# Performance work log

Hardware: AMD Instinct MI355X
Metric: run time of the kernel (lower is better)

The kernel has to match this reference:

```python
import jax, jax.numpy as jnp
import numpy as np

K = 100  # low-rank dimension


def setup_inputs() -> dict:
    key = jax.random.key(0)
    k1, k2 = jax.random.split(key)
    N, D = 100000, 512
    X = jax.random.normal(k1, (N, D), dtype=jnp.float32)
    # xavier-normal init for Linear(d, 4k): std = sqrt(2/(fan_in+fan_out))
    std = np.sqrt(2.0 / (D + 4 * K)).astype(np.float32)
    W = jax.random.normal(k2, (4 * K, D), dtype=jnp.float32) * std
    b = jnp.zeros((4 * K,), dtype=jnp.float32)
    return {"X": X, "W": W, "b": b}


def reference(X, W, b):
    # tmp = ReLU(X @ W^T + b): [N, 4k]
    tmp = jax.nn.relu(X @ W.T + b)
    U = tmp[:, :K]            # [N, k]
    V = tmp[:, K:2 * K]       # [N, k]
    Z = tmp[:, 2 * K:3 * K]   # [N, k]
    T = tmp[:, 3 * K:]        # [N, k]
    N_rows = X.shape[0]
    # joint_normalize2: sum(U @ (V^T @ ones)) / N + 1e-6 == <colsum(U), colsum(V)> / N + 1e-6
    norm_factor = jnp.dot(jnp.sum(U, axis=0), jnp.sum(V, axis=0)) / N_rows + 1e-6
    Dscale = 1.0 / norm_factor
    # low-rank attention: U @ (V^T @ Z) via small [k, k] intermediate
    VtZ = jnp.einsum('nk,nj->kj', V, Z)   # [k, k]
    res = (U @ VtZ) * Dscale              # [N, k]
    out = jnp.concatenate([res, T], axis=1)  # [N, 2k]
    # dropout p=0.0 (eval-equivalent): identity
    return out
```

## Files before the change

kernel.cpp:

```cpp
#include <hip/hip_runtime.h>
#include <cstdint>

typedef __bf16 bf16;
typedef __attribute__((ext_vector_type(8))) __bf16 bf16x8;
typedef __attribute__((ext_vector_type(4))) __bf16 bf16x4;
typedef __attribute__((ext_vector_type(4))) float f32x4;

#define NROWS 100000
#define DIM   512
#define NC    400
#define NTILE 695

#define WS_WP    0u
#define WS_SUMU  458752u
#define WS_SUMV  459152u
#define WS_DSC   459552u
#define WS_VTZT  459776u
#define WS_U     524288u
#define WS_PART  66124288u
#define WS_SUMP  71041536u
#define WS_NEED  72291936u

__device__ __forceinline__ void gload_lds16(const void* g, void* l) {
  __builtin_amdgcn_global_load_lds(
      (const __attribute__((address_space(1))) uint32_t*)g,
      (__attribute__((address_space(3))) uint32_t*)l,
      16, 0, 0);
}

__global__ void k1_prep(const float* __restrict__ W, bf16* __restrict__ wp,
                        float* __restrict__ sums) {
  const int idx = blockIdx.x * 256 + threadIdx.x;
  if (idx < 200) sums[idx] = 0.f;
  if (idx >= 16 * 4 * 448 * 8) return;
  const int e = idx & 7;
  int r = idx >> 3;
  const int col = r % 448; r /= 448;
  const int g = r & 3;
  const int t = r >> 2;
  const int k = t * 32 + 4 * g + ((e < 4) ? e : (12 + e));
  wp[idx] = (bf16)((col < NC) ? W[col * DIM + k] : 0.f);
}

__global__ __launch_bounds__(768, 3) void k2_main(
    const float* __restrict__ X, const bf16* __restrict__ Wp,
    const float* __restrict__ bias, float* __restrict__ out,
    bf16* __restrict__ U, float* __restrict__ part, float* __restrict__ sumP) {
  __shared__ __align__(16) char pool[141312];
  char* Abase0 = pool;
  char* Bbase0 = pool + 55296;

  const int tid  = threadIdx.x;
  const int lane = tid & 63;
  const int wave = tid >> 6;
  const int wm = wave >> 2;
  const int wn = wave & 3;
  const int m  = lane & 15;
  const int g  = lane >> 4;
  const int rb = blockIdx.x * 144;

  f32x4 acc[3][7];
#pragma unroll
  for (int i = 0; i < 3; ++i)
#pragma unroll
    for (int j = 0; j < 7; ++j) acc[i][j] = (f32x4){0.f, 0.f, 0.f, 0.f};

  const int na  = (wave < 6) ? 2 : 1;
  const int ca0 = (wave < 6) ? wave * 2 : 12 + (wave - 6);
  const size_t swb = (size_t)(((lane & 7) ^ (lane >> 3)) * 16);
  int gr0 = rb + ca0 * 8 + (lane >> 3);       if (gr0 > NROWS - 1) gr0 = NROWS - 1;
  int gr1 = rb + (ca0 + 1) * 8 + (lane >> 3); if (gr1 > NROWS - 1) gr1 = NROWS - 1;
  const char* asrc0 = (const char*)X + (size_t)gr0 * 2048 + swb;
  const char* asrc1 = (const char*)X + (size_t)gr1 * 2048 + swb;
  const int nbc = (wave < 4) ? 3 : 2;
  const int bc0 = (wave < 4) ? wave * 3 : 12 + (wave - 4) * 2;
  const char* wpc = (const char*)Wp;

#define STAGE(T, BUF)                                                          \
  do {                                                                         \
    char* ad = Abase0 + (BUF) * 18432 + ca0 * 1024 + lane * 16;                \
    gload_lds16(asrc0 + (size_t)(T) * 128, ad);                                \
    if (na == 2) gload_lds16(asrc1 + (size_t)(T) * 128, ad + 1024);            \
    const char* bsrc = wpc + (size_t)(T) * 28672;                              \
    for (int q = 0; q < nbc; ++q)                                              \
      gload_lds16(bsrc + (bc0 + q) * 1024 + lane * 16,                         \
                  Bbase0 + (BUF) * 28672 + (bc0 + q) * 1024);                  \
  } while (0)

  STAGE(0, 0);
  STAGE(1, 1);

#pragma unroll
  for (int t = 0; t < 16; ++t) {
    const int cur = t % 3;
    if (t < 15) {
      if (wave < 4)      asm volatile("s_waitcnt vmcnt(5)\n\ts_barrier" ::: "memory");
      else if (wave < 6) asm volatile("s_waitcnt vmcnt(4)\n\ts_barrier" ::: "memory");
      else               asm volatile("s_waitcnt vmcnt(3)\n\ts_barrier" ::: "memory");
    } else {
      asm volatile("s_waitcnt vmcnt(0)\n\ts_barrier" ::: "memory");
    }
    if (t + 2 < 16) STAGE(t + 2, (t + 2) % 3);

    const int sw = (m & 7) * 16;
    const char* abuf = Abase0 + cur * 18432;
    bf16x8 af[3];
#pragma unroll
    for (int mf = 0; mf < 3; ++mf) {
      const char* rowp = abuf + (wm * 48 + mf * 16 + m) * 128;
      f32x4 alo = *(const f32x4*)(rowp + ((16 * g) ^ sw));
      f32x4 ahi = *(const f32x4*)(rowp + ((64 + 16 * g) ^ sw));
      af[mf] = (bf16x8){(bf16)alo.x, (bf16)alo.y, (bf16)alo.z, (bf16)alo.w,
                        (bf16)ahi.x, (bf16)ahi.y, (bf16)ahi.z, (bf16)ahi.w};
    }

    const bf16* Bc = (const bf16*)(Bbase0 + cur * 28672);
    __builtin_amdgcn_s_setprio(1);
#pragma unroll
    for (int nf = 0; nf < 7; ++nf) {
      const int n = wn * 112 + nf * 16 + m;
      bf16x8 bfr = *(const bf16x8*)(Bc + (g * 448 + n) * 8);
#pragma unroll
      for (int mf = 0; mf < 3; ++mf)
        acc[mf][nf] = __builtin_amdgcn_mfma_f32_16x16x32_bf16(af[mf], bfr, acc[mf][nf], 0, 0, 0);
    }
    __builtin_amdgcn_s_setprio(0);
  }
#undef STAGE
  __syncthreads();

  bf16* ldsVZ = (bf16*)pool;
  float* sp   = (float*)(pool + 75264);
  float csum[7];
#pragma unroll
  for (int nf = 0; nf < 7; ++nf) csum[nf] = 0.f;

#pragma unroll
  for (int mf = 0; mf < 3; ++mf) {
#pragma unroll
    for (int nf = 0; nf < 7; ++nf) {
      const int c = wn * 112 + nf * 16 + m;
      const float bv = (c < NC) ? bias[c] : 0.f;
      const int rl0 = wm * 48 + mf * 16 + 4 * g;
      bf16 vz[4];
#pragma unroll
      for (int r = 0; r < 4; ++r) {
        const int row = rb + rl0 + r;
        float v = fmaxf(acc[mf][nf][r] + bv, 0.f);
        const float v2 = (row < NROWS) ? v : 0.f;
        if (row < NROWS) {
          if (c < 100) U[(size_t)row * 128 + c] = (bf16)v;
          if (c >= 300 && c < NC) out[(size_t)row * 200 + 100 + (c - 300)] = v;
        }
        vz[r] = (bf16)v2;
        if (c < 200) csum[nf] += v2;
      }
      if (c >= 100 && c < 300) {
        const int vr = (c < 200) ? (c - 100) : (112 + (c - 200));
        *(bf16x4*)&ldsVZ[(size_t)vr * 168 + rl0] = (bf16x4){vz[0], vz[1], vz[2], vz[3]};
      }
    }
  }
  for (int i = tid; i < 8832; i += 768) {
    int rr, cc;
    if (i < 5376) { rr = i / 24; cc = 144 + (i % 24); }
    else { const int j = i - 5376; const int q = j / 144; cc = j % 144;
           rr = (q < 12) ? (100 + q) : (200 + q); }
    ldsVZ[(size_t)rr * 168 + cc] = (bf16)0.f;
  }
#pragma unroll
  for (int nf = 0; nf < 7; ++nf) {
    float s = csum[nf];
    s += __shfl_xor(s, 16, 64);
    s += __shfl_xor(s, 32, 64);
    if (lane < 16) sp[wave * 112 + nf * 16 + lane] = s;
  }
  __syncthreads();

  if (wave < 7) {
    f32x4 acc2[7];
#pragma unroll
    for (int j = 0; j < 7; ++j) acc2[j] = (f32x4){0.f, 0.f, 0.f, 0.f};
    const bf16* vA = ldsVZ + (size_t)(wave * 16 + m) * 168;
#pragma unroll
    for (int kc = 0; kc < 5; ++kc) {
      bf16x4 a0 = *(const bf16x4*)(vA + kc * 32 + 4 * g);
      bf16x4 a1 = *(const bf16x4*)(vA + kc * 32 + 16 + 4 * g);
      bf16x8 af_ = {a0[0], a0[1], a0[2], a0[3], a1[0], a1[1], a1[2], a1[3]};
#pragma unroll
      for (int fj = 0; fj < 7; ++fj) {
        const bf16* vB = ldsVZ + (size_t)(112 + fj * 16 + m) * 168 + kc * 32;
        bf16x4 b0 = *(const bf16x4*)(vB + 4 * g);
        bf16x4 b1 = *(const bf16x4*)(vB + 16 + 4 * g);
        bf16x8 bf_ = {b0[0], b0[1], b0[2], b0[3], b1[0], b1[1], b1[2], b1[3]};
        acc2[fj] = __builtin_amdgcn_mfma_f32_16x16x32_bf16(af_, bf_, acc2[fj], 0, 0, 0);
      }
    }
    float* pb = part + (size_t)(blockIdx.x % 98) * 12544;
#pragma unroll
    for (int fj = 0; fj < 7; ++fj)
#pragma unroll
      for (int r = 0; r < 4; ++r)
        atomicAdd(&pb[(wave * 16 + 4 * g + r) * 112 + fj * 16 + m], acc2[fj][r]);
  }
  if (tid < 200) {
    const int wq = tid / 112, cc = tid % 112;
    sumP[(size_t)blockIdx.x * 200 + tid] =
        sp[(0 * 4 + wq) * 112 + cc] + sp[(1 * 4 + wq) * 112 + cc] +
        sp[(2 * 4 + wq) * 112 + cc];
  }
}

__global__ void k4a0_redsum(const float* __restrict__ sumP,
                            float* __restrict__ sumU, float* __restrict__ sumV) {
  __shared__ float red[4];
  const int c = blockIdx.x;
  const int tid = threadIdx.x;
  float s = 0.f;
  for (int b = tid; b < NTILE; b += 256) s += sumP[(size_t)b * 200 + c];
#pragma unroll
  for (int off = 1; off < 64; off <<= 1) s += __shfl_xor(s, off, 64);
  if ((tid & 63) == 0) red[tid >> 6] = s;
  __syncthreads();
  if (tid == 0) {
    float t = red[0] + red[1] + red[2] + red[3];
    if (c < 100) sumU[c] = t; else sumV[c - 100] = t;
  }
}

__global__ void k4a_norm(const float* __restrict__ sumU, const float* __restrict__ sumV,
                         float* __restrict__ dsc) {
  const int l = threadIdx.x;
  float v = 0.f;
  if (l < 50) v = sumU[l] * sumV[l] + sumU[l + 50] * sumV[l + 50];
#pragma unroll
  for (int off = 32; off > 0; off >>= 1) v += __shfl_down(v, off, 64);
  if (l == 0) dsc[0] = 1.f / (v * (1.f / (float)NROWS) + 1e-6f);
}

__global__ void k4b_final(const float* __restrict__ part, const float* __restrict__ dsc,
                          bf16* __restrict__ vtzt) {
  const int idx = blockIdx.x * 256 + threadIdx.x;
  if (idx < 1792) vtzt[(idx >> 4) * 128 + 112 + (idx & 15)] = (bf16)0.f;
  if (idx >= 12544) return;
  const int i = idx / 112;
  const int j = idx % 112;
  float s = 0.f;
#pragma unroll 7
  for (int bb = 0; bb < 98; ++bb) s += part[(size_t)bb * 12544 + idx];
  vtzt[j * 128 + i] = (bf16)(s * dsc[0]);
}

__global__ __launch_bounds__(256) void k5_res(
    const bf16* __restrict__ U, const bf16* __restrict__ vtzt,
    float* __restrict__ out) {
  const int tid = threadIdx.x;
  const int lane = tid & 63;
  const int wave = tid >> 6;
  const int m = lane & 15, g = lane >> 4;
  const int rb = blockIdx.x * 128 + wave * 32;

  f32x4 acc[2][7];
#pragma unroll
  for (int i = 0; i < 2; ++i)
#pragma unroll
    for (int j = 0; j < 7; ++j) acc[i][j] = (f32x4){0.f, 0.f, 0.f, 0.f};

  int r0 = rb + m;      if (r0 > NROWS - 1) r0 = NROWS - 1;
  int r1 = rb + 16 + m; if (r1 > NROWS - 1) r1 = NROWS - 1;
  const bf16* u0 = U + (size_t)r0 * 128 + 4 * g;
  const bf16* u1 = U + (size_t)r1 * 128 + 4 * g;
  const bf16* vb = vtzt + 4 * g;

#pragma unroll
  for (int ks = 0; ks < 4; ++ks) {
    bf16x4 A00 = *(const bf16x4*)(u0 + ks * 32);
    bf16x4 A01 = *(const bf16x4*)(u0 + ks * 32 + 16);
    bf16x4 A10 = *(const bf16x4*)(u1 + ks * 32);
    bf16x4 A11 = *(const bf16x4*)(u1 + ks * 32 + 16);
    bf16x8 af0 = {A00[0], A00[1], A00[2], A00[3], A01[0], A01[1], A01[2], A01[3]};
    bf16x8 af1 = {A10[0], A10[1], A10[2], A10[3], A11[0], A11[1], A11[2], A11[3]};
#pragma unroll
    for (int nf = 0; nf < 7; ++nf) {
      const int n = nf * 16 + m;
      bf16x4 B0 = *(const bf16x4*)(vb + n * 128 + ks * 32);
      bf16x4 B1 = *(const bf16x4*)(vb + n * 128 + ks * 32 + 16);
      bf16x8 bfr = {B0[0], B0[1], B0[2], B0[3], B1[0], B1[1], B1[2], B1[3]};
      acc[0][nf] = __builtin_amdgcn_mfma_f32_16x16x32_bf16(af0, bfr, acc[0][nf], 0, 0, 0);
      acc[1][nf] = __builtin_amdgcn_mfma_f32_16x16x32_bf16(af1, bfr, acc[1][nf], 0, 0, 0);
    }
  }
#pragma unroll
  for (int mf = 0; mf < 2; ++mf)
#pragma unroll
    for (int nf = 0; nf < 7; ++nf)
#pragma unroll
      for (int r = 0; r < 4; ++r) {
        const int row = rb + mf * 16 + 4 * g + r;
        const int c = nf * 16 + m;
        if (row < NROWS && c < 100)
          out[(size_t)row * 200 + c] = acc[mf][nf][r];
      }
}

extern "C" void kernel_launch(void* const* d_in, const int* in_sizes, int n_in,
                              void* d_out, int out_size, void* d_ws, size_t ws_size,
                              hipStream_t stream) {
  const float* X = (const float*)d_in[0];
  const float* W = (const float*)d_in[1];
  const float* b = (const float*)d_in[2];
  float* out = (float*)d_out;
  char* ws = (char*)d_ws;
  if (ws_size < WS_NEED) return;

  bf16* wp     = (bf16*)(ws + WS_WP);
  float* sumU  = (float*)(ws + WS_SUMU);
  float* sumV  = (float*)(ws + WS_SUMV);
  float* dsc   = (float*)(ws + WS_DSC);
  bf16* vtzt   = (bf16*)(ws + WS_VTZT);
  bf16* U      = (bf16*)(ws + WS_U);
  float* part  = (float*)(ws + WS_PART);
  float* sumP  = (float*)(ws + WS_SUMP);

  k1_prep<<<896, 256, 0, stream>>>(W, wp, sumU);
  hipMemsetAsync(part, 0, 98u * 12544u * 4u, stream);
  k2_main<<<NTILE, 768, 0, stream>>>(X, wp, b, out, U, part, sumP);
  k4a0_redsum<<<200, 256, 0, stream>>>(sumP, sumU, sumV);
  k4a_norm<<<1, 64, 0, stream>>>(sumU, sumV, dsc);
  k4b_final<<<49, 256, 0, stream>>>(part, dsc, vtzt);
  k5_res<<<782, 256, 0, stream>>>(U, vtzt, out);
}
```

Measured before the change: 174.1 us.

## Load X tiles directly into registers instead of staging through LDS

The A operand (X rows) is now read straight from global memory into registers with inline global_load_dwordx4, double-buffered one k-step ahead, instead of being staged through LDS with global_load_lds and a triple buffer. This removes the A LDS buffers and their read traffic, cutting shared memory from about 138KB to 84KB, and changes the vmcnt wait counts to match. The trade-off is higher register pressure (12 extra f32x4 per thread) at 768 threads per block. Direct per-lane global loads may also coalesce less well than the staged path, since each lane reads 16B pieces of different rows. The pool must still be large enough for the epilogue's use of it.

Measured after the change: 246.7 us. 41.7% more time.

```diff
diff --git a/kernel.cpp b/kernel.cpp
--- a/kernel.cpp
+++ b/kernel.cpp
@@ -46,9 +46,8 @@
     const float* __restrict__ X, const bf16* __restrict__ Wp,
     const float* __restrict__ bias, float* __restrict__ out,
     bf16* __restrict__ U, float* __restrict__ part, float* __restrict__ sumP) {
-  __shared__ __align__(16) char pool[141312];
-  char* Abase0 = pool;
-  char* Bbase0 = pool + 55296;
+  __shared__ __align__(16) char pool[86016];
+  char* Bbase0 = pool;
 
   const int tid  = threadIdx.x;
   const int lane = tid & 63;
@@ -65,53 +64,64 @@
 #pragma unroll
     for (int j = 0; j < 7; ++j) acc[i][j] = (f32x4){0.f, 0.f, 0.f, 0.f};
 
-  const int na  = (wave < 6) ? 2 : 1;
-  const int ca0 = (wave < 6) ? wave * 2 : 12 + (wave - 6);
-  const size_t swb = (size_t)(((lane & 7) ^ (lane >> 3)) * 16);
-  int gr0 = rb + ca0 * 8 + (lane >> 3);       if (gr0 > NROWS - 1) gr0 = NROWS - 1;
-  int gr1 = rb + (ca0 + 1) * 8 + (lane >> 3); if (gr1 > NROWS - 1) gr1 = NROWS - 1;
-  const char* asrc0 = (const char*)X + (size_t)gr0 * 2048 + swb;
-  const char* asrc1 = (const char*)X + (size_t)gr1 * 2048 + swb;
+  const char* rp[3];
+#pragma unroll
+  for (int mf = 0; mf < 3; ++mf) {
+    int row = rb + wm * 48 + mf * 16 + m;
+    if (row > NROWS - 1) row = NROWS - 1;
+    rp[mf] = (const char*)X + (size_t)row * 2048 + g * 16;
+  }
   const int nbc = (wave < 4) ? 3 : 2;
   const int bc0 = (wave < 4) ? wave * 3 : 12 + (wave - 4) * 2;
   const char* wpc = (const char*)Wp;
 
-#define STAGE(T, BUF)                                                          \
+#define STAGE_B(T, BUF)                                                        \
   do {                                                                         \
-    char* ad = Abase0 + (BUF) * 18432 + ca0 * 1024 + lane * 16;                \
-    gload_lds16(asrc0 + (size_t)(T) * 128, ad);                                \
-    if (na == 2) gload_lds16(asrc1 + (size_t)(T) * 128, ad + 1024);            \
     const char* bsrc = wpc + (size_t)(T) * 28672;                              \
     for (int q = 0; q < nbc; ++q)                                              \
       gload_lds16(bsrc + (bc0 + q) * 1024 + lane * 16,                         \
                   Bbase0 + (BUF) * 28672 + (bc0 + q) * 1024);                  \
   } while (0)
 
-  STAGE(0, 0);
-  STAGE(1, 1);
+#define ALOAD(T, B_)                                                           \
+  do {                                                                         \
+    _Pragma("unroll")                                                          \
+    for (int mf = 0; mf < 3; ++mf) {                                           \
+      asm volatile("global_load_dwordx4 %0, %1, off"                           \
+                   : "=v"(Ar[B_][2 * mf])                                      \
+                   : "v"(rp[mf] + (size_t)(T) * 128) : "memory");              \
+      asm volatile("global_load_dwordx4 %0, %1, off"                           \
+                   : "=v"(Ar[B_][2 * mf + 1])                                  \
+                   : "v"(rp[mf] + (size_t)(T) * 128 + 64) : "memory");         \
+    }                                                                          \
+  } while (0)
+
+  f32x4 Ar[2][6];
+  STAGE_B(0, 0);
+  ALOAD(0, 0);
+  STAGE_B(1, 1);
 
 #pragma unroll
   for (int t = 0; t < 16; ++t) {
     const int cur = t % 3;
     if (t < 15) {
-      if (wave < 4)      asm volatile("s_waitcnt vmcnt(5)\n\ts_barrier" ::: "memory");
-      else if (wave < 6) asm volatile("s_waitcnt vmcnt(4)\n\ts_barrier" ::: "memory");
-      else               asm volatile("s_waitcnt vmcnt(3)\n\ts_barrier" ::: "memory");
+      if (wave < 4) asm volatile("s_waitcnt vmcnt(3)\n\ts_barrier" ::: "memory");
+      else          asm volatile("s_waitcnt vmcnt(2)\n\ts_barrier" ::: "memory");
     } else {
       asm volatile("s_waitcnt vmcnt(0)\n\ts_barrier" ::: "memory");
     }
-    if (t + 2 < 16) STAGE(t + 2, (t + 2) % 3);
-
-    const int sw = (m & 7) * 16;
-    const char* abuf = Abase0 + cur * 18432;
+    __builtin_amdgcn_sched_barrier(0);
+
+    if (t + 1 < 16) ALOAD(t + 1, (t + 1) & 1);
+    if (t + 2 < 16) STAGE_B(t + 2, (t + 2) % 3);
+
     bf16x8 af[3];
 #pragma unroll
     for (int mf = 0; mf < 3; ++mf) {
-      const char* rowp = abuf + (wm * 48 + mf * 16 + m) * 128;
-      f32x4 alo = *(const f32x4*)(rowp + ((16 * g) ^ sw));
-      f32x4 ahi = *(const f32x4*)(rowp + ((64 + 16 * g) ^ sw));
-      af[mf] = (bf16x8){(bf16)alo.x, (bf16)alo.y, (bf16)alo.z, (bf16)alo.w,
-                        (bf16)ahi.x, (bf16)ahi.y, (bf16)ahi.z, (bf16)ahi.w};
+      f32x4 lo = Ar[t & 1][2 * mf];
+      f32x4 hi = Ar[t & 1][2 * mf + 1];
+      af[mf] = (bf16x8){(bf16)lo.x, (bf16)lo.y, (bf16)lo.z, (bf16)lo.w,
+                        (bf16)hi.x, (bf16)hi.y, (bf16)hi.z, (bf16)hi.w};
     }
 
     const bf16* Bc = (const bf16*)(Bbase0 + cur * 28672);
@@ -126,7 +136,8 @@
     }
     __builtin_amdgcn_s_setprio(0);
   }
-#undef STAGE
+#undef STAGE_B
+#undef ALOAD
   __syncthreads();
 
   bf16* ldsVZ = (bf16*)pool;
```
